# Performance work log

Hardware: AMD Instinct MI355X
Metric: run time of the kernel (lower is better)

The kernel has to match this reference:

```python
import jax, jax.numpy as jnp
import numpy as np

HIDDEN = 256

def setup_inputs() -> dict:
    key = jax.random.key(0)
    k1, k2, k3, k4, k5, k6 = jax.random.split(key, 6)
    s = 1.0 / np.sqrt(HIDDEN)
    return {
        "queries": jax.random.normal(k1, (4, 200, HIDDEN), dtype=jnp.float32),
        "mask_features": jax.random.normal(k2, (4, HIDDEN, 256, 256), dtype=jnp.float32),
        "w1": jax.random.uniform(k3, (HIDDEN, HIDDEN), jnp.float32, -s, s),
        "b1": jax.random.uniform(k4, (HIDDEN,), jnp.float32, -s, s),
        "w2": jax.random.uniform(k5, (HIDDEN, HIDDEN), jnp.float32, -s, s),
        "b2": jax.random.uniform(k6, (HIDDEN,), jnp.float32, -s, s),
    }

def reference(queries, mask_features, w1, b1, w2, b2):
    # mask_embed = Linear -> ReLU -> Linear  (per-query MLP)
    h = jax.nn.relu(jnp.einsum('bqc,dc->bqd', queries, w1) + b1)
    mask_embed = jnp.einsum('bqd,cd->bqc', h, w2) + b2  # (B, Q, C)
    # dot over channels: equivalent to broadcast-multiply-sum in the original
    pred_masks = jnp.einsum('bqc,bchw->bqhw', mask_embed, mask_features)
    return pred_masks
```

## Files before the change

kernel.cpp:

```cpp
#include <hip/hip_runtime.h>
#include <hip/hip_bf16.h>

#define HIDDEN 256
#define NB 4
#define NQ 200
#define MT 13
#define HW 65536
#define KSTEPS 8
#define NPB 64
#define NTILE 16
#define GT 512
#define HBB 16384
#define ABYTES (MT * KSTEPS * 1024)
#define SMEM_TOTAL (ABYTES + 3 * HBB)

typedef __attribute__((ext_vector_type(8))) __bf16 bf16x8;
typedef __attribute__((ext_vector_type(4))) float f32x4;

#define WAITVM0()    asm volatile("s_waitcnt vmcnt(0)" ::: "memory")
#define WAIT_LGKM0() asm volatile("s_waitcnt lgkmcnt(0)" ::: "memory")
__device__ __forceinline__ void hard_barrier() {
    __builtin_amdgcn_sched_barrier(0);
    __builtin_amdgcn_s_barrier();
    __builtin_amdgcn_sched_barrier(0);
}

__device__ __forceinline__ void gload_lds16(const void* g, void* l) {
    __builtin_amdgcn_global_load_lds(
        (const __attribute__((address_space(1))) void*)g,
        (__attribute__((address_space(3))) void*)l, 16, 0, 0);
}

__global__ __launch_bounds__(1024)
void mlp_pack(const float* __restrict__ queries,
              const float* __restrict__ w1, const float* __restrict__ b1,
              const float* __restrict__ w2, const float* __restrict__ b2,
              __bf16* __restrict__ A_ws)
{
    __shared__ float qh[16][HIDDEN];
    __shared__ float wb[HIDDEN][33];
    const int blk = blockIdx.x;
    const int b = blk / MT, mt = blk % MT;
    const int tid = threadIdx.x;

    for (int idx = tid; idx < 16 * HIDDEN; idx += 1024) {
        int r = idx >> 8, c = idx & 255;
        int q = mt * 16 + r;
        qh[r][c] = (q < NQ) ? queries[((size_t)b * NQ + q) * HIDDEN + c] : 0.f;
    }
    __syncthreads();

    const int t  = tid & 255;
    const int rq = tid >> 8;
    const int sr = tid >> 2;
    const int si = tid & 3;

    float h[4];
    #pragma unroll
    for (int r = 0; r < 4; ++r) h[r] = b1[t];
    for (int cc = 0; cc < 8; ++cc) {
        const float* src = w1 + (size_t)sr * HIDDEN + cc * 32;
        float4 va = *reinterpret_cast<const float4*>(src + si * 4);
        float4 vb = *reinterpret_cast<const float4*>(src + 16 + si * 4);
        wb[sr][si*4+0] = va.x; wb[sr][si*4+1] = va.y;
        wb[sr][si*4+2] = va.z; wb[sr][si*4+3] = va.w;
        wb[sr][16+si*4+0] = vb.x; wb[sr][16+si*4+1] = vb.y;
        wb[sr][16+si*4+2] = vb.z; wb[sr][16+si*4+3] = vb.w;
        __syncthreads();
        #pragma unroll
        for (int cl = 0; cl < 32; ++cl) {
            float w = wb[t][cl];
            #pragma unroll
            for (int r = 0; r < 4; ++r)
                h[r] = fmaf(qh[rq * 4 + r][cc * 32 + cl], w, h[r]);
        }
        __syncthreads();
    }

    #pragma unroll
    for (int r = 0; r < 4; ++r) qh[rq * 4 + r][t] = fmaxf(h[r], 0.f);
    __syncthreads();

    float me[4];
    #pragma unroll
    for (int r = 0; r < 4; ++r) me[r] = b2[t];
    for (int cc = 0; cc < 8; ++cc) {
        const float* src = w2 + (size_t)sr * HIDDEN + cc * 32;
        float4 va = *reinterpret_cast<const float4*>(src + si * 4);
        float4 vb = *reinterpret_cast<const float4*>(src + 16 + si * 4);
        wb[sr][si*4+0] = va.x; wb[sr][si*4+1] = va.y;
        wb[sr][si*4+2] = va.z; wb[sr][si*4+3] = va.w;
        wb[sr][16+si*4+0] = vb.x; wb[sr][16+si*4+1] = vb.y;
        wb[sr][16+si*4+2] = vb.z; wb[sr][16+si*4+3] = vb.w;
        __syncthreads();
        #pragma unroll
        for (int cl = 0; cl < 32; ++cl) {
            float w = wb[t][cl];
            #pragma unroll
            for (int r = 0; r < 4; ++r)
                me[r] = fmaf(qh[rq * 4 + r][cc * 32 + cl], w, me[r]);
        }
        __syncthreads();
    }

    const int ks = t >> 5, g = (t >> 3) & 3, j = t & 7;
    #pragma unroll
    for (int r = 0; r < 4; ++r) {
        int row = rq * 4 + r;
        int q = mt * 16 + row;
        float v = (q < NQ) ? me[r] : 0.f;
        int lane = row + 16 * g;
        size_t addr = ((size_t)((b * MT + mt) * KSTEPS + ks)) * 512 + (size_t)lane * 8 + j;
        A_ws[addr] = (__bf16)v;
    }
}

__global__ __launch_bounds__(GT)
void mask_gemm(const float* __restrict__ mf,
               const __bf16* __restrict__ A_ws,
               float* __restrict__ out)
{
    extern __shared__ char smem[];
    char* Ar = smem;
    char* HB = smem + ABYTES;

    const int bid = blockIdx.x;
    const int b   = bid >> 6;
    const int px0 = (bid & 63) * (NTILE * NPB);
    const int tid = threadIdx.x;
    const int ln  = tid & 63, wv = tid >> 6;
    const int l15 = ln & 15,  lg = ln >> 4;
    const bool has2 = (wv + 8) < MT;
    const int sn = ln;
    const int su = wv;

    const float*  mfB  = mf  + (size_t)b * HIDDEN * HW;
    const __bf16* Ab   = A_ws + (size_t)b * (MT * KSTEPS * 512);
    float*        outB = out + (size_t)b * NQ * HW;

    for (int fi = wv; fi < MT * KSTEPS; fi += 8)
        gload_lds16(Ab + (size_t)fi * 512 + (size_t)ln * 8,
                    Ar + fi * 1024 + ln * 16);

    float v[16];
    {
        const float* src = mfB + px0 + sn;
        #pragma unroll
        for (int c = 0; c < 2; ++c)
            #pragma unroll
            for (int j = 0; j < 8; ++j)
                v[c * 8 + j] = src[(size_t)((su * 2 + c) * 8 + j) * HW];
    }
    WAITVM0();
    #pragma unroll
    for (int c = 0; c < 2; ++c) {
        bf16x8 pk;
        #pragma unroll
        for (int j = 0; j < 8; ++j) pk[j] = (__bf16)v[c * 8 + j];
        const int u = su * 2 + c;
        *reinterpret_cast<bf16x8*>(HB + sn * 256 + ((u ^ (sn & 7)) << 4)) = pk;
    }
    WAIT_LGKM0();
    hard_barrier();

    f32x4 acc[2][4];
    #pragma unroll
    for (int ii = 0; ii < 2; ++ii)
        #pragma unroll
        for (int f = 0; f < 4; ++f) acc[ii][f] = (f32x4){0.f, 0.f, 0.f, 0.f};

    for (int s = 0; s < 2 * NTILE; ++s) {
        const int i = s >> 1, h = s & 1;
        char* bcur = HB + (s % 3) * HBB;
        const bool hn = (s + 1) < 2 * NTILE;

        if (hn) {
            const int i2 = (s + 1) >> 1, h2 = (s + 1) & 1;
            const float* src = mfB + (size_t)h2 * 128 * HW + px0 + i2 * NPB + sn;
            #pragma unroll
            for (int c = 0; c < 2; ++c)
                #pragma unroll
                for (int j = 0; j < 8; ++j)
                    v[c * 8 + j] = src[(size_t)((su * 2 + c) * 8 + j) * HW];
            __builtin_amdgcn_sched_barrier(0);
        }

        #pragma unroll
        for (int kk = 0; kk < 4; ++kk) {
            const int t = h * 4 + kk;
            bf16x8 a0 = *reinterpret_cast<const bf16x8*>(
                Ar + (wv * KSTEPS + t) * 1024 + ln * 16);
            bf16x8 a1;
            if (has2)
                a1 = *reinterpret_cast<const bf16x8*>(
                    Ar + ((wv + 8) * KSTEPS + t) * 1024 + ln * 16);
            #pragma unroll
            for (int f = 0; f < 4; ++f) {
                bf16x8 bf = *reinterpret_cast<const bf16x8*>(
                    bcur + (f * 16 + l15) * 256 + (((kk * 4 + lg) ^ (l15 & 7)) << 4));
                acc[0][f] = __builtin_amdgcn_mfma_f32_16x16x32_bf16(
                    a0, bf, acc[0][f], 0, 0, 0);
                if (has2)
                    acc[1][f] = __builtin_amdgcn_mfma_f32_16x16x32_bf16(
                        a1, bf, acc[1][f], 0, 0, 0);
            }
        }

        if (hn) {
            char* bnxt = HB + ((s + 1) % 3) * HBB;
            #pragma unroll
            for (int c = 0; c < 2; ++c) {
                bf16x8 pk;
                #pragma unroll
                for (int j = 0; j < 8; ++j) pk[j] = (__bf16)v[c * 8 + j];
                const int u = su * 2 + c;
                *reinterpret_cast<bf16x8*>(bnxt + sn * 256 + ((u ^ (sn & 7)) << 4)) = pk;
            }
        }

        if (h == 1) {
            float* wscr = reinterpret_cast<float*>(
                HB + ((s + 2) % 3) * HBB + wv * 2048);
            const int n0 = px0 + i * NPB;
            #pragma unroll
            for (int ii = 0; ii < 2; ++ii) {
                if (ii == 0 || has2) {
                    const int mt = wv + 8 * ii;
                    #pragma unroll
                    for (int sp = 0; sp < 4; ++sp) {
                        if (lg == sp) {
                            #pragma unroll
                            for (int f = 0; f < 4; ++f)
                                #pragma unroll
                                for (int r = 0; r < 4; ++r)
                                    wscr[r * 64 + f * 16 + l15] = acc[ii][f][r];
                        }
                        WAIT_LGKM0();
                        {
                            const int row = ln >> 4, c4 = (ln & 15) << 2;
                            f32x4 vv = *reinterpret_cast<const f32x4*>(
                                wscr + row * 64 + c4);
                            const int q = mt * 16 + sp * 4 + row;
                            if (q < NQ)
                                __builtin_nontemporal_store(vv,
                                    reinterpret_cast<f32x4*>(
                                        outB + (size_t)q * HW + n0 + c4));
                        }
                        WAIT_LGKM0();
                    }
                }
            }
            #pragma unroll
            for (int ii = 0; ii < 2; ++ii)
                #pragma unroll
                for (int f = 0; f < 4; ++f)
                    acc[ii][f] = (f32x4){0.f, 0.f, 0.f, 0.f};
        }

        WAIT_LGKM0();
        hard_barrier();
    }
}

extern "C" void kernel_launch(void* const* d_in, const int* in_sizes, int n_in,
                              void* d_out, int out_size, void* d_ws, size_t ws_size,
                              hipStream_t stream)
{
    const float* queries = (const float*)d_in[0];
    const float* mf      = (const float*)d_in[1];
    const float* w1      = (const float*)d_in[2];
    const float* b1      = (const float*)d_in[3];
    const float* w2      = (const float*)d_in[4];
    const float* b2      = (const float*)d_in[5];
    float*  out  = (float*)d_out;
    __bf16* A_ws = (__bf16*)d_ws;

    (void)hipFuncSetAttribute((const void*)mask_gemm,
                              hipFuncAttributeMaxDynamicSharedMemorySize,
                              SMEM_TOTAL);

    hipLaunchKernelGGL(mlp_pack, dim3(NB * MT), dim3(1024), 0, stream,
                       queries, w1, b1, w2, b2, A_ws);
    hipLaunchKernelGGL(mask_gemm, dim3(256), dim3(GT), SMEM_TOTAL, stream,
                       mf, A_ws, out);
}
```

Measured before the change: 131.4 us.

## Deepen mask-feature register prefetch to two stages with an unrolled loop

The main loop is unrolled by two half-tiles, and two register buffers (vA, vB) hold global loads of mask features issued two stages ahead instead of one. Each half-tile's bf16 LDS write happens while the other buffer's load is still in flight, which is meant to hide more HBM latency in this memory-bound GEMM that runs one block per CU. The cost is extra VGPR pressure from the second 16-float buffer, and the LDS buffer indexing is rearranged to keep the triple buffering and the epilogue scratch slot consistent.

```diff
diff --git a/kernel.cpp b/kernel.cpp
--- a/kernel.cpp
+++ b/kernel.cpp
@@ -142,24 +142,39 @@
         gload_lds16(Ab + (size_t)fi * 512 + (size_t)ln * 8,
                     Ar + fi * 1024 + ln * 16);
 
-    float v[16];
-    {
-        const float* src = mfB + px0 + sn;
-        #pragma unroll
-        for (int c = 0; c < 2; ++c)
-            #pragma unroll
-            for (int j = 0; j < 8; ++j)
-                v[c * 8 + j] = src[(size_t)((su * 2 + c) * 8 + j) * HW];
-    }
+    float vA[16], vB[16];
+
+    #define LOADV(dst, slot)                                                   \
+        do {                                                                   \
+            const int i_ = (slot) >> 1, h_ = (slot) & 1;                       \
+            const float* src_ = mfB + (size_t)h_ * 128 * HW                    \
+                                + px0 + i_ * NPB + sn;                         \
+            _Pragma("unroll")                                                  \
+            for (int c_ = 0; c_ < 2; ++c_)                                     \
+                _Pragma("unroll")                                              \
+                for (int j_ = 0; j_ < 8; ++j_)                                 \
+                    dst[c_ * 8 + j_] =                                         \
+                        src_[(size_t)((su * 2 + c_) * 8 + j_) * HW];           \
+        } while (0)
+
+    #define DSWRITE(base, srcv)                                                \
+        do {                                                                   \
+            _Pragma("unroll")                                                  \
+            for (int c_ = 0; c_ < 2; ++c_) {                                   \
+                bf16x8 pk_;                                                    \
+                _Pragma("unroll")                                              \
+                for (int j_ = 0; j_ < 8; ++j_)                                 \
+                    pk_[j_] = (__bf16)srcv[c_ * 8 + j_];                       \
+                const int u_ = su * 2 + c_;                                    \
+                *reinterpret_cast<bf16x8*>(                                    \
+                    (base) + sn * 256 + ((u_ ^ (sn & 7)) << 4)) = pk_;         \
+            }                                                                  \
+        } while (0)
+
+    LOADV(vA, 0);
+    LOADV(vB, 1);
     WAITVM0();
-    #pragma unroll
-    for (int c = 0; c < 2; ++c) {
-        bf16x8 pk;
-        #pragma unroll
-        for (int j = 0; j < 8; ++j) pk[j] = (__bf16)v[c * 8 + j];
-        const int u = su * 2 + c;
-        *reinterpret_cast<bf16x8*>(HB + sn * 256 + ((u ^ (sn & 7)) << 4)) = pk;
-    }
+    DSWRITE(HB, vA);
     WAIT_LGKM0();
     hard_barrier();
 
@@ -169,58 +184,54 @@
         #pragma unroll
         for (int f = 0; f < 4; ++f) acc[ii][f] = (f32x4){0.f, 0.f, 0.f, 0.f};
 
-    for (int s = 0; s < 2 * NTILE; ++s) {
-        const int i = s >> 1, h = s & 1;
-        char* bcur = HB + (s % 3) * HBB;
-        const bool hn = (s + 1) < 2 * NTILE;
-
-        if (hn) {
-            const int i2 = (s + 1) >> 1, h2 = (s + 1) & 1;
-            const float* src = mfB + (size_t)h2 * 128 * HW + px0 + i2 * NPB + sn;
-            #pragma unroll
-            for (int c = 0; c < 2; ++c)
-                #pragma unroll
-                for (int j = 0; j < 8; ++j)
-                    v[c * 8 + j] = src[(size_t)((su * 2 + c) * 8 + j) * HW];
+    #define COMPUTE(bcur, hh)                                                  \
+        do {                                                                   \
+            _Pragma("unroll")                                                  \
+            for (int kk = 0; kk < 4; ++kk) {                                   \
+                const int t_ = (hh) * 4 + kk;                                  \
+                bf16x8 a0 = *reinterpret_cast<const bf16x8*>(                  \
+                    Ar + (wv * KSTEPS + t_) * 1024 + ln * 16);                 \
+                bf16x8 a1;                                                     \
+                if (has2)                                                      \
+                    a1 = *reinterpret_cast<const bf16x8*>(                     \
+                        Ar + ((wv + 8) * KSTEPS + t_) * 1024 + ln * 16);       \
+                _Pragma("unroll")                                              \
+                for (int f = 0; f < 4; ++f) {                                  \
+                    bf16x8 bf = *reinterpret_cast<const bf16x8*>(              \
+                        (bcur) + (f * 16 + l15) * 256                          \
+                        + (((kk * 4 + lg) ^ (l15 & 7)) << 4));                 \
+                    acc[0][f] = __builtin_amdgcn_mfma_f32_16x16x32_bf16(       \
+                        a0, bf, acc[0][f], 0, 0, 0);                           \
+                    if (has2)                                                  \
+                        acc[1][f] = __builtin_amdgcn_mfma_f32_16x16x32_bf16(   \
+                            a1, bf, acc[1][f], 0, 0, 0);                       \
+                }                                                              \
+            }                                                                  \
+        } while (0)
+
+    for (int i = 0; i < NTILE; ++i) {
+        const int s0 = 2 * i;
+
+        if (s0 + 2 < 2 * NTILE) {
+            LOADV(vA, s0 + 2);
             __builtin_amdgcn_sched_barrier(0);
         }
-
-        #pragma unroll
-        for (int kk = 0; kk < 4; ++kk) {
-            const int t = h * 4 + kk;
-            bf16x8 a0 = *reinterpret_cast<const bf16x8*>(
-                Ar + (wv * KSTEPS + t) * 1024 + ln * 16);
-            bf16x8 a1;
-            if (has2)
-                a1 = *reinterpret_cast<const bf16x8*>(
-                    Ar + ((wv + 8) * KSTEPS + t) * 1024 + ln * 16);
-            #pragma unroll
-            for (int f = 0; f < 4; ++f) {
-                bf16x8 bf = *reinterpret_cast<const bf16x8*>(
-                    bcur + (f * 16 + l15) * 256 + (((kk * 4 + lg) ^ (l15 & 7)) << 4));
-                acc[0][f] = __builtin_amdgcn_mfma_f32_16x16x32_bf16(
-                    a0, bf, acc[0][f], 0, 0, 0);
-                if (has2)
-                    acc[1][f] = __builtin_amdgcn_mfma_f32_16x16x32_bf16(
-                        a1, bf, acc[1][f], 0, 0, 0);
-            }
-        }
-
-        if (hn) {
-            char* bnxt = HB + ((s + 1) % 3) * HBB;
-            #pragma unroll
-            for (int c = 0; c < 2; ++c) {
-                bf16x8 pk;
-                #pragma unroll
-                for (int j = 0; j < 8; ++j) pk[j] = (__bf16)v[c * 8 + j];
-                const int u = su * 2 + c;
-                *reinterpret_cast<bf16x8*>(bnxt + sn * 256 + ((u ^ (sn & 7)) << 4)) = pk;
-            }
-        }
-
-        if (h == 1) {
+        COMPUTE(HB + (s0 % 3) * HBB, 0);
+        DSWRITE(HB + ((s0 + 1) % 3) * HBB, vB);
+        WAIT_LGKM0();
+        hard_barrier();
+
+        if (s0 + 3 < 2 * NTILE) {
+            LOADV(vB, s0 + 3);
+            __builtin_amdgcn_sched_barrier(0);
+        }
+        COMPUTE(HB + ((s0 + 1) % 3) * HBB, 1);
+        if (s0 + 2 < 2 * NTILE)
+            DSWRITE(HB + ((s0 + 2) % 3) * HBB, vA);
+
+        {
             float* wscr = reinterpret_cast<float*>(
-                HB + ((s + 2) % 3) * HBB + wv * 2048);
+                HB + (s0 % 3) * HBB + wv * 2048);
             const int n0 = px0 + i * NPB;
             #pragma unroll
             for (int ii = 0; ii < 2; ++ii) {
@@ -260,6 +271,9 @@
         WAIT_LGKM0();
         hard_barrier();
     }
+    #undef LOADV
+    #undef DSWRITE
+    #undef COMPUTE
 }
 
 extern "C" void kernel_launch(void* const* d_in, const int* in_sizes, int n_in,
@@ -281,6 +295,6 @@
 
     hipLaunchKernelGGL(mlp_pack, dim3(NB * MT), dim3(1024), 0, stream,
                        queries, w1, b1, w2, b2, A_ws);
-    hipLaunchKernelGGL(mask_gemm, dim3(256), dim3(GT), SMEM_TOTAL, stream,
+    hipLaunchKernelGGL(mask_gemm, dim3(NB * 64), dim3(GT), SMEM_TOTAL, stream,
                        mf, A_ws, out);
 }
```

New measurement: 127.3 us. -3.1%, faster.

## Widen pixel tile to 128 and pipeline K in quarter slices

Applied to the files above, without the earlier changes.

Doubles the pixel tile per iteration from 64 to 128 columns and splits the 256-channel reduction into four 64-channel slices. Each slice is staged through the triple-buffered LDS, so there are 32 pipeline steps instead of 32 half-steps over a narrower tile. The global load pattern changes so each wave reads 8 channel rows across 128 contiguous pixels, which gives wider coalesced rows, and each staged B fragment is reused across 8 MFMA column tiles. The cost is twice as many accumulator registers and a wider epilogue, which may lower occupancy or cause spills.

```diff
diff --git a/kernel.cpp b/kernel.cpp
--- a/kernel.cpp
+++ b/kernel.cpp
@@ -7,8 +7,9 @@
 #define MT 13
 #define HW 65536
 #define KSTEPS 8
-#define NPB 64
-#define NTILE 16
+#define NPB 128
+#define NTILE 8
+#define NSLOT 32
 #define GT 512
 #define HBB 16384
 #define ABYTES (MT * KSTEPS * 1024)
@@ -131,8 +132,6 @@
     const int ln  = tid & 63, wv = tid >> 6;
     const int l15 = ln & 15,  lg = ln >> 4;
     const bool has2 = (wv + 8) < MT;
-    const int sn = ln;
-    const int su = wv;
 
     const float*  mfB  = mf  + (size_t)b * HIDDEN * HW;
     const __bf16* Ab   = A_ws + (size_t)b * (MT * KSTEPS * 512);
@@ -143,61 +142,69 @@
                     Ar + fi * 1024 + ln * 16);
 
     float v[16];
-    {
-        const float* src = mfB + px0 + sn;
-        #pragma unroll
-        for (int c = 0; c < 2; ++c)
-            #pragma unroll
-            for (int j = 0; j < 8; ++j)
-                v[c * 8 + j] = src[(size_t)((su * 2 + c) * 8 + j) * HW];
-    }
+
+    #define LOADV(dst, slot)                                                   \
+        do {                                                                   \
+            const int i_ = (slot) >> 2, kq_ = (slot) & 3;                      \
+            const float* src_ = mfB + (size_t)(kq_ * 64 + wv * 8) * HW         \
+                                + px0 + i_ * NPB;                              \
+            _Pragma("unroll")                                                  \
+            for (int j_ = 0; j_ < 8; ++j_)                                     \
+                _Pragma("unroll")                                              \
+                for (int c_ = 0; c_ < 2; ++c_)                                 \
+                    dst[c_ * 8 + j_] =                                         \
+                        src_[(size_t)j_ * HW + c_ * 64 + ln];                  \
+        } while (0)
+
+    #define DSWRITE(base, srcv)                                                \
+        do {                                                                   \
+            _Pragma("unroll")                                                  \
+            for (int c_ = 0; c_ < 2; ++c_) {                                   \
+                bf16x8 pk_;                                                    \
+                _Pragma("unroll")                                              \
+                for (int j_ = 0; j_ < 8; ++j_)                                 \
+                    pk_[j_] = (__bf16)srcv[c_ * 8 + j_];                       \
+                const int n_ = c_ * 64 + ln;                                   \
+                *reinterpret_cast<bf16x8*>(                                    \
+                    (base) + n_ * 128 + ((wv ^ (n_ & 7)) << 4)) = pk_;         \
+            }                                                                  \
+        } while (0)
+
+    LOADV(v, 0);
     WAITVM0();
-    #pragma unroll
-    for (int c = 0; c < 2; ++c) {
-        bf16x8 pk;
-        #pragma unroll
-        for (int j = 0; j < 8; ++j) pk[j] = (__bf16)v[c * 8 + j];
-        const int u = su * 2 + c;
-        *reinterpret_cast<bf16x8*>(HB + sn * 256 + ((u ^ (sn & 7)) << 4)) = pk;
-    }
+    DSWRITE(HB, v);
     WAIT_LGKM0();
     hard_barrier();
 
-    f32x4 acc[2][4];
+    f32x4 acc[2][8];
     #pragma unroll
     for (int ii = 0; ii < 2; ++ii)
         #pragma unroll
-        for (int f = 0; f < 4; ++f) acc[ii][f] = (f32x4){0.f, 0.f, 0.f, 0.f};
-
-    for (int s = 0; s < 2 * NTILE; ++s) {
-        const int i = s >> 1, h = s & 1;
+        for (int f = 0; f < 8; ++f) acc[ii][f] = (f32x4){0.f, 0.f, 0.f, 0.f};
+
+    for (int s = 0; s < NSLOT; ++s) {
+        const int i = s >> 2, kq = s & 3;
         char* bcur = HB + (s % 3) * HBB;
-        const bool hn = (s + 1) < 2 * NTILE;
+        const bool hn = (s + 1) < NSLOT;
 
         if (hn) {
-            const int i2 = (s + 1) >> 1, h2 = (s + 1) & 1;
-            const float* src = mfB + (size_t)h2 * 128 * HW + px0 + i2 * NPB + sn;
-            #pragma unroll
-            for (int c = 0; c < 2; ++c)
-                #pragma unroll
-                for (int j = 0; j < 8; ++j)
-                    v[c * 8 + j] = src[(size_t)((su * 2 + c) * 8 + j) * HW];
+            LOADV(v, s + 1);
             __builtin_amdgcn_sched_barrier(0);
         }
 
         #pragma unroll
-        for (int kk = 0; kk < 4; ++kk) {
-            const int t = h * 4 + kk;
+        for (int t = 0; t < 2; ++t) {
+            const int t_ = kq * 2 + t;
             bf16x8 a0 = *reinterpret_cast<const bf16x8*>(
-                Ar + (wv * KSTEPS + t) * 1024 + ln * 16);
+                Ar + (wv * KSTEPS + t_) * 1024 + ln * 16);
             bf16x8 a1;
             if (has2)
                 a1 = *reinterpret_cast<const bf16x8*>(
-                    Ar + ((wv + 8) * KSTEPS + t) * 1024 + ln * 16);
-            #pragma unroll
-            for (int f = 0; f < 4; ++f) {
+                    Ar + ((wv + 8) * KSTEPS + t_) * 1024 + ln * 16);
+            #pragma unroll
+            for (int f = 0; f < 8; ++f) {
                 bf16x8 bf = *reinterpret_cast<const bf16x8*>(
-                    bcur + (f * 16 + l15) * 256 + (((kk * 4 + lg) ^ (l15 & 7)) << 4));
+                    bcur + (f * 16 + l15) * 128 + (((t * 4 + lg) ^ (l15 & 7)) << 4));
                 acc[0][f] = __builtin_amdgcn_mfma_f32_16x16x32_bf16(
                     a0, bf, acc[0][f], 0, 0, 0);
                 if (has2)
@@ -206,19 +213,10 @@
             }
         }
 
-        if (hn) {
-            char* bnxt = HB + ((s + 1) % 3) * HBB;
-            #pragma unroll
-            for (int c = 0; c < 2; ++c) {
-                bf16x8 pk;
-                #pragma unroll
-                for (int j = 0; j < 8; ++j) pk[j] = (__bf16)v[c * 8 + j];
-                const int u = su * 2 + c;
-                *reinterpret_cast<bf16x8*>(bnxt + sn * 256 + ((u ^ (sn & 7)) << 4)) = pk;
-            }
-        }
-
-        if (h == 1) {
+        if (hn)
+            DSWRITE(HB + ((s + 1) % 3) * HBB, v);
+
+        if (kq == 3) {
             float* wscr = reinterpret_cast<float*>(
                 HB + ((s + 2) % 3) * HBB + wv * 2048);
             const int n0 = px0 + i * NPB;
@@ -230,16 +228,18 @@
                     for (int sp = 0; sp < 4; ++sp) {
                         if (lg == sp) {
                             #pragma unroll
-                            for (int f = 0; f < 4; ++f)
+                            for (int f = 0; f < 8; ++f)
                                 #pragma unroll
                                 for (int r = 0; r < 4; ++r)
-                                    wscr[r * 64 + f * 16 + l15] = acc[ii][f][r];
+                                    wscr[r * 128 + f * 16 + l15] = acc[ii][f][r];
                         }
                         WAIT_LGKM0();
-                        {
-                            const int row = ln >> 4, c4 = (ln & 15) << 2;
+                        #pragma unroll
+                        for (int rp = 0; rp < 2; ++rp) {
+                            const int row = rp * 2 + (ln >> 5);
+                            const int c4 = (ln & 31) << 2;
                             f32x4 vv = *reinterpret_cast<const f32x4*>(
-                                wscr + row * 64 + c4);
+                                wscr + row * 128 + c4);
                             const int q = mt * 16 + sp * 4 + row;
                             if (q < NQ)
                                 __builtin_nontemporal_store(vv,
@@ -253,13 +253,15 @@
             #pragma unroll
             for (int ii = 0; ii < 2; ++ii)
                 #pragma unroll
-                for (int f = 0; f < 4; ++f)
+                for (int f = 0; f < 8; ++f)
                     acc[ii][f] = (f32x4){0.f, 0.f, 0.f, 0.f};
         }
 
         WAIT_LGKM0();
         hard_barrier();
     }
+    #undef LOADV
+    #undef DSWRITE
 }
 
 extern "C" void kernel_launch(void* const* d_in, const int* in_sizes, int n_in,
@@ -281,6 +283,6 @@
 
     hipLaunchKernelGGL(mlp_pack, dim3(NB * MT), dim3(1024), 0, stream,
                        queries, w1, b1, w2, b2, A_ws);
-    hipLaunchKernelGGL(mask_gemm, dim3(256), dim3(GT), SMEM_TOTAL, stream,
+    hipLaunchKernelGGL(mask_gemm, dim3(NB * 64), dim3(GT), SMEM_TOTAL, stream,
                        mf, A_ws, out);
 }
```

Measured after the change: 130.8 us. About the same (-0.5%).
